# Optimization experiments

Measured on AMD Instinct MI355X. Metric: run time of the kernel, lower is better.

Reference implementation:

```python
import jax, jax.numpy as jnp
import numpy as np

INP = 64   # inplanes
PLN = 64   # planes
LOC = 64   # loc_planes
EPS = 1e-5


def _linear_init(key, fan_in, fan_out):
    # torch nn.Linear default: U(-1/sqrt(fan_in), 1/sqrt(fan_in)) for W and b
    kw, kb = jax.random.split(key)
    bound = 1.0 / np.sqrt(fan_in)
    W = jax.random.uniform(kw, (fan_in, fan_out), jnp.float32, -bound, bound)
    b = jax.random.uniform(kb, (fan_out,), jnp.float32, -bound, bound)
    return W, b


def setup_inputs() -> dict:
    key = jax.random.key(0)
    ks = jax.random.split(key, 8)
    B, N = 8, 4096
    img_fea = jax.random.normal(ks[0], (B, N, INP), jnp.float32)
    loc_fea = jax.random.normal(ks[1], (B, N, LOC), jnp.float32)
    W11, b11 = _linear_init(ks[2], INP + LOC, INP)
    W12, b12 = _linear_init(ks[3], INP, INP)
    W21, b21 = _linear_init(ks[4], INP + LOC, INP)
    W22, b22 = _linear_init(ks[5], INP, INP * PLN)
    W3, b3 = _linear_init(ks[6], PLN, PLN)
    ln_g = jnp.ones((PLN,), jnp.float32)
    ln_b = jnp.zeros((PLN,), jnp.float32)
    return {
        "img_fea": img_fea, "loc_fea": loc_fea,
        "W11": W11, "b11": b11, "W12": W12, "b12": b12,
        "W21": W21, "b21": b21, "W22": W22, "b22": b22,
        "ln_g": ln_g, "ln_b": ln_b, "W3": W3, "b3": b3,
    }


def reference(img_fea, loc_fea, W11, b11, W12, b12, W21, b21, W22, b22,
              ln_g, ln_b, W3, b3):
    B, N, C = img_fea.shape
    cat_fea = jnp.concatenate([img_fea, loc_fea], axis=2)  # [B,N,INP+LOC]
    # branch 1: per-token input vector
    w11 = jax.nn.relu(cat_fea @ W11 + b11)                 # [B,N,INP]
    w12 = w11 @ W12 + b12                                  # [B,N,INP]
    # branch 2: per-token weight matrix generation
    w21 = jax.nn.relu(cat_fea @ W21 + b21)                 # [B,N,INP]
    w22 = (w21 @ W22 + b22).reshape(B, N, INP, PLN)        # [B,N,INP,PLN]
    # batched tiny matvec: (1,INP) @ (INP,PLN) per token
    x = jnp.einsum('bni,bnio->bno', w12, w22)              # [B,N,PLN]
    # LayerNorm over last dim + ReLU
    mu = jnp.mean(x, axis=-1, keepdims=True)
    var = jnp.mean(jnp.square(x - mu), axis=-1, keepdims=True)
    x = (x - mu) * jax.lax.rsqrt(var + EPS) * ln_g + ln_b
    x = jax.nn.relu(x)
    # final linear (no activation)
    return x @ W3 + b3
```

## Files before the change

### kernel.cpp

```cpp
#include <hip/hip_runtime.h>
#include <cstdint>


typedef __bf16 bf16x8 __attribute__((ext_vector_type(8)));
typedef float  f32x4  __attribute__((ext_vector_type(4)));
typedef float  f32x8  __attribute__((ext_vector_type(8)));

#define MFMA16(A, B, C) __builtin_amdgcn_mfma_f32_16x16x32_bf16(A, B, C, 0, 0, 0)

#define OFF_BT22 0
#define OFF_W11  266240
#define OFF_W21  274432
#define OFF_W12  282624
#define OFF_W3   286720
#define WS_ELEMS 290816

__global__ __launch_bounds__(256) void prep_kernel(
    const float* __restrict__ W22, const float* __restrict__ b22,
    const float* __restrict__ W11, const float* __restrict__ W21,
    const float* __restrict__ W12, const float* __restrict__ W3,
    __bf16* __restrict__ ws)
{
    int gid = blockIdx.x * 256 + threadIdx.x;
    const float* src = nullptr; const float* srcb = nullptr;
    int base;
    if (gid < OFF_W11)      { base = OFF_BT22; src = W22; srcb = b22; }
    else if (gid < OFF_W12) { base = (gid < OFF_W21) ? OFF_W11 : OFF_W21;
                              src  = (gid < OFF_W21) ? W11 : W21; }
    else if (gid < OFF_W3)  { base = OFF_W12; src = W12; }
    else                    { base = OFF_W3;  src = W3;  }
    int d = gid - base;
    int kb = d >> 9, o = (d >> 3) & 63, kj = d & 7;
    int k = kb * 8 + kj;
    float v = (srcb && k >= 4096) ? srcb[(k - 4096) * 64 + o] : src[k * 64 + o];
    ws[gid] = (__bf16)v;
}

__global__ __launch_bounds__(256, 1) void main_kernel(
    const float* __restrict__ img, const float* __restrict__ loc,
    const float* __restrict__ b11, const float* __restrict__ b12,
    const float* __restrict__ b21, const float* __restrict__ ln_g,
    const float* __restrict__ ln_b, const float* __restrict__ b3,
    const __bf16* __restrict__ ws, float* __restrict__ out)
{
    __shared__ __align__(1024) char smem[90112];
    __bf16* catL = (__bf16*)smem;
    __bf16* w11L = (__bf16*)(smem + 34816);
    __bf16* w21L = (__bf16*)(smem + 53248);
    __bf16* w12L = (__bf16*)(smem + 71680);

    const int tid  = threadIdx.x;
    const int wv   = tid >> 6;
    const int lane = tid & 63;
    const int ln   = lane & 15;
    const int quad = lane >> 4;
    const int wt   = wv * 32;
    const long tb  = (long)blockIdx.x * 128;

    const __bf16* Bt22  = ws + OFF_BT22;
    const __bf16* W11bt = ws + OFF_W11;
    const __bf16* W21bt = ws + OFF_W21;
    const __bf16* W12bt = ws + OFF_W12;
    const __bf16* W3bt  = ws + OFF_W3;

    {
        const float* srcs[2] = {img, loc};
        #pragma unroll
        for (int s = 0; s < 2; ++s) {
            const float* src = srcs[s] + tb * 64;
            #pragma unroll
            for (int it = 0; it < 8; ++it) {
                int u = (it * 256 + tid) * 4;
                int t = u >> 6, c = u & 63;
                const float4 v = *(const float4*)(src + u);
                __bf16* p = catL + t * 136 + s * 64 + c;
                p[0] = (__bf16)v.x; p[1] = (__bf16)v.y;
                p[2] = (__bf16)v.z; p[3] = (__bf16)v.w;
            }
        }
    }
    __syncthreads();

    {
        f32x4 a11[2][4] = {}; f32x4 a21[2][4] = {};
        #pragma unroll
        for (int kb = 0; kb < 4; ++kb) {
            bf16x8 af[2];
            #pragma unroll
            for (int mf = 0; mf < 2; ++mf)
                af[mf] = *(const bf16x8*)(catL + (wt + mf*16 + ln)*136 + kb*32 + quad*8);
            #pragma unroll
            for (int nf = 0; nf < 4; ++nf) {
                int o = nf*16 + ln;
                bf16x8 bw1 = *(const bf16x8*)(W11bt + ((kb*4 + quad)*64 + o)*8);
                bf16x8 bw2 = *(const bf16x8*)(W21bt + ((kb*4 + quad)*64 + o)*8);
                #pragma unroll
                for (int mf = 0; mf < 2; ++mf) {
                    a11[mf][nf] = MFMA16(af[mf], bw1, a11[mf][nf]);
                    a21[mf][nf] = MFMA16(af[mf], bw2, a21[mf][nf]);
                }
            }
        }
        #pragma unroll
        for (int nf = 0; nf < 4; ++nf) {
            int o = nf*16 + ln;
            float c11 = b11[o], c21 = b21[o];
            #pragma unroll
            for (int mf = 0; mf < 2; ++mf)
                #pragma unroll
                for (int r = 0; r < 4; ++r) {
                    int t = wt + mf*16 + quad*4 + r;
                    float v1 = a11[mf][nf][r] + c11; v1 = v1 > 0.f ? v1 : 0.f;
                    float v2 = a21[mf][nf][r] + c21; v2 = v2 > 0.f ? v2 : 0.f;
                    w11L[t*72 + o] = (__bf16)v1;
                    w21L[t*72 + o] = (__bf16)v2;
                }
        }
    }
    __syncthreads();

    auto stage = [&](int c) {
        const int ng = (c == 32) ? 8 : 16;
        char* buf = smem + (c & 1) * 16384;
        for (int g = wv; g < ng; g += 4) {
            const __bf16* gsrc = Bt22 + ((long)(c*16 + g) * 512) + lane * 8;
            void* ldst = buf + g * 1024;
            __builtin_amdgcn_global_load_lds(
                (const __attribute__((address_space(1))) uint32_t*)gsrc,
                (__attribute__((address_space(3))) uint32_t*)ldst, 16, 0, 0);
        }
    };
    stage(0);

    {
        f32x4 a12c[2][4] = {};
        #pragma unroll
        for (int kb = 0; kb < 2; ++kb) {
            bf16x8 af[2];
            #pragma unroll
            for (int mf = 0; mf < 2; ++mf)
                af[mf] = *(const bf16x8*)(w11L + (wt + mf*16 + ln)*72 + kb*32 + quad*8);
            #pragma unroll
            for (int nf = 0; nf < 4; ++nf) {
                bf16x8 bw = *(const bf16x8*)(W12bt + ((kb*4 + quad)*64 + nf*16 + ln)*8);
                #pragma unroll
                for (int mf = 0; mf < 2; ++mf)
                    a12c[mf][nf] = MFMA16(af[mf], bw, a12c[mf][nf]);
            }
        }
        #pragma unroll
        for (int nf = 0; nf < 4; ++nf) {
            int o = nf*16 + ln;
            float c12 = b12[o];
            #pragma unroll
            for (int mf = 0; mf < 2; ++mf)
                #pragma unroll
                for (int r = 0; r < 4; ++r) {
                    int t = wt + mf*16 + quad*4 + r;
                    w12L[t*72 + o] = (__bf16)(a12c[mf][nf][r] + c12);
                }
        }
    }
    __syncthreads();

    bf16x8 a12[2][2]; f32x8 w12f[2][2];
    #pragma unroll
    for (int mf = 0; mf < 2; ++mf)
        #pragma unroll
        for (int sub = 0; sub < 2; ++sub) {
            a12[mf][sub]  = *(const bf16x8*)(w12L + (wt + mf*16 + ln)*72 + sub*32 + quad*8);
            w12f[mf][sub] = __builtin_convertvector(a12[mf][sub], f32x8);
        }

    f32x4 acc[2][4] = {};
    for (int c = 0; c <= 32; ++c) {
        if (c < 32) stage(c + 1);
        const __bf16* buf = (const __bf16*)(smem + (c & 1) * 16384);
        if (c < 32) {
            #pragma unroll
            for (int kbl = 0; kbl < 4; ++kbl) {
                int j = c*2 + (kbl >> 1), sub = kbl & 1;
                bf16x8 af[2];
                #pragma unroll
                for (int mf = 0; mf < 2; ++mf) {
                    float wj = (float)w21L[(wt + mf*16 + ln)*72 + j];
                    af[mf] = __builtin_convertvector(w12f[mf][sub] * wj, bf16x8);
                }
                #pragma unroll
                for (int nf = 0; nf < 4; ++nf) {
                    bf16x8 bfr = *(const bf16x8*)(buf + (kbl*4 + quad)*512 + (nf*16 + ln)*8);
                    #pragma unroll
                    for (int mf = 0; mf < 2; ++mf)
                        acc[mf][nf] = MFMA16(af[mf], bfr, acc[mf][nf]);
                }
            }
        } else {
            #pragma unroll
            for (int kbl = 0; kbl < 2; ++kbl)
                #pragma unroll
                for (int nf = 0; nf < 4; ++nf) {
                    bf16x8 bfr = *(const bf16x8*)(buf + (kbl*4 + quad)*512 + (nf*16 + ln)*8);
                    #pragma unroll
                    for (int mf = 0; mf < 2; ++mf)
                        acc[mf][nf] = MFMA16(a12[mf][kbl], bfr, acc[mf][nf]);
                }
        }
        __syncthreads();
    }

    float gv[4], bv[4], b3v[4];
    #pragma unroll
    for (int nf = 0; nf < 4; ++nf) {
        int o = nf*16 + ln;
        gv[nf] = ln_g[o]; bv[nf] = ln_b[o]; b3v[nf] = b3[o];
    }
    __bf16* xL = w11L;
    #pragma unroll
    for (int mf = 0; mf < 2; ++mf)
        #pragma unroll
        for (int r = 0; r < 4; ++r) {
            float s1 = 0.f, s2 = 0.f;
            #pragma unroll
            for (int nf = 0; nf < 4; ++nf) { float v = acc[mf][nf][r]; s1 += v; s2 += v*v; }
            #pragma unroll
            for (int d = 1; d < 16; d <<= 1) {
                s1 += __shfl_xor(s1, d, 64);
                s2 += __shfl_xor(s2, d, 64);
            }
            float mean = s1 * 0.015625f;
            float var  = s2 * 0.015625f - mean * mean;
            float inv  = rsqrtf(var + 1e-5f);
            int t = wt + mf*16 + quad*4 + r;
            #pragma unroll
            for (int nf = 0; nf < 4; ++nf) {
                float v = (acc[mf][nf][r] - mean) * inv * gv[nf] + bv[nf];
                v = v > 0.f ? v : 0.f;
                xL[t*72 + nf*16 + ln] = (__bf16)v;
            }
        }
    __syncthreads();

    f32x4 a3[2][4] = {};
    #pragma unroll
    for (int kb = 0; kb < 2; ++kb) {
        bf16x8 af[2];
        #pragma unroll
        for (int mf = 0; mf < 2; ++mf)
            af[mf] = *(const bf16x8*)(xL + (wt + mf*16 + ln)*72 + kb*32 + quad*8);
        #pragma unroll
        for (int nf = 0; nf < 4; ++nf) {
            bf16x8 bfr = *(const bf16x8*)(W3bt + ((kb*4 + quad)*64 + nf*16 + ln)*8);
            #pragma unroll
            for (int mf = 0; mf < 2; ++mf)
                a3[mf][nf] = MFMA16(af[mf], bfr, a3[mf][nf]);
        }
    }
    #pragma unroll
    for (int mf = 0; mf < 2; ++mf)
        #pragma unroll
        for (int nf = 0; nf < 4; ++nf)
            #pragma unroll
            for (int r = 0; r < 4; ++r) {
                long t = tb + wt + mf*16 + quad*4 + r;
                out[t*64 + nf*16 + ln] = a3[mf][nf][r] + b3v[nf];
            }
}

extern "C" void kernel_launch(void* const* d_in, const int* in_sizes, int n_in,
                              void* d_out, int out_size, void* d_ws, size_t ws_size,
                              hipStream_t stream)
{
    const float* img  = (const float*)d_in[0];
    const float* loc  = (const float*)d_in[1];
    const float* W11  = (const float*)d_in[2];
    const float* b11  = (const float*)d_in[3];
    const float* W12  = (const float*)d_in[4];
    const float* b12  = (const float*)d_in[5];
    const float* W21  = (const float*)d_in[6];
    const float* b21  = (const float*)d_in[7];
    const float* W22  = (const float*)d_in[8];
    const float* b22  = (const float*)d_in[9];
    const float* ln_g = (const float*)d_in[10];
    const float* ln_b = (const float*)d_in[11];
    const float* W3   = (const float*)d_in[12];
    const float* b3   = (const float*)d_in[13];
    __bf16* ws = (__bf16*)d_ws;
    float*  o  = (float*)d_out;

    prep_kernel<<<1136, 256, 0, stream>>>(W22, b22, W11, W21, W12, W3, ws);
    main_kernel<<<256, 256, 0, stream>>>(img, loc, b11, b12, b21, ln_g, ln_b, b3, ws, o);
}
```

Baseline: 134.9 us.

## Double W22 staging chunk size, tile prep transpose via LDS, vectorize stores

New measurement: 133.0 us. Within noise of the previous version (-1.3%).

```diff
diff --git a/kernel.cpp b/kernel.cpp
--- a/kernel.cpp
+++ b/kernel.cpp
@@ -2,6 +2,7 @@
 #include <cstdint>
 
 
+typedef __bf16 bf16x4 __attribute__((ext_vector_type(4)));
 typedef __bf16 bf16x8 __attribute__((ext_vector_type(8)));
 typedef float  f32x4  __attribute__((ext_vector_type(4)));
 typedef float  f32x8  __attribute__((ext_vector_type(8)));
@@ -13,7 +14,6 @@
 #define OFF_W21  274432
 #define OFF_W12  282624
 #define OFF_W3   286720
-#define WS_ELEMS 290816
 
 __global__ __launch_bounds__(256) void prep_kernel(
     const float* __restrict__ W22, const float* __restrict__ b22,
@@ -21,19 +21,33 @@
     const float* __restrict__ W12, const float* __restrict__ W3,
     __bf16* __restrict__ ws)
 {
-    int gid = blockIdx.x * 256 + threadIdx.x;
-    const float* src = nullptr; const float* srcb = nullptr;
-    int base;
-    if (gid < OFF_W11)      { base = OFF_BT22; src = W22; srcb = b22; }
-    else if (gid < OFF_W12) { base = (gid < OFF_W21) ? OFF_W11 : OFF_W21;
-                              src  = (gid < OFF_W21) ? W11 : W21; }
-    else if (gid < OFF_W3)  { base = OFF_W12; src = W12; }
-    else                    { base = OFF_W3;  src = W3;  }
-    int d = gid - base;
-    int kb = d >> 9, o = (d >> 3) & 63, kj = d & 7;
-    int k = kb * 8 + kj;
-    float v = (srcb && k >= 4096) ? srcb[(k - 4096) * 64 + o] : src[k * 64 + o];
-    ws[gid] = (__bf16)v;
+    __shared__ __bf16 T[64][72];
+    const int b = blockIdx.x, tid = threadIdx.x;
+    const float* src; __bf16* dst;
+    if (b < 64)       { src = W22 + b * 4096;        dst = ws + OFF_BT22 + b * 4096; }
+    else if (b == 64) { src = b22;                   dst = ws + OFF_BT22 + 64 * 4096; }
+    else if (b < 67)  { src = W11 + (b - 65) * 4096; dst = ws + OFF_W11 + (b - 65) * 4096; }
+    else if (b < 69)  { src = W21 + (b - 67) * 4096; dst = ws + OFF_W21 + (b - 67) * 4096; }
+    else if (b == 69) { src = W12;                   dst = ws + OFF_W12; }
+    else              { src = W3;                    dst = ws + OFF_W3; }
+    #pragma unroll
+    for (int it = 0; it < 4; ++it) {
+        int u = it * 1024 + tid * 4;
+        int r = u >> 6, c = u & 63;
+        const float4 v = *(const float4*)(src + u);
+        T[r][c] = (__bf16)v.x; T[r][c + 1] = (__bf16)v.y;
+        T[r][c + 2] = (__bf16)v.z; T[r][c + 3] = (__bf16)v.w;
+    }
+    __syncthreads();
+    #pragma unroll
+    for (int it = 0; it < 2; ++it) {
+        int item = it * 256 + tid;
+        int q = item >> 6, o = item & 63;
+        bf16x8 pk;
+        #pragma unroll
+        for (int kj = 0; kj < 8; ++kj) pk[kj] = T[q * 8 + kj][o];
+        *(bf16x8*)(dst + q * 512 + o * 8) = pk;
+    }
 }
 
 __global__ __launch_bounds__(256, 1) void main_kernel(
@@ -43,11 +57,11 @@
     const float* __restrict__ ln_b, const float* __restrict__ b3,
     const __bf16* __restrict__ ws, float* __restrict__ out)
 {
-    __shared__ __align__(1024) char smem[90112];
+    __shared__ __align__(1024) char smem[102400];
     __bf16* catL = (__bf16*)smem;
     __bf16* w11L = (__bf16*)(smem + 34816);
-    __bf16* w21L = (__bf16*)(smem + 53248);
-    __bf16* w12L = (__bf16*)(smem + 71680);
+    __bf16* w21L = (__bf16*)(smem + 65536);
+    __bf16* w12L = (__bf16*)(smem + 83968);
 
     const int tid  = threadIdx.x;
     const int wv   = tid >> 6;
@@ -73,9 +87,8 @@
                 int u = (it * 256 + tid) * 4;
                 int t = u >> 6, c = u & 63;
                 const float4 v = *(const float4*)(src + u);
-                __bf16* p = catL + t * 136 + s * 64 + c;
-                p[0] = (__bf16)v.x; p[1] = (__bf16)v.y;
-                p[2] = (__bf16)v.z; p[3] = (__bf16)v.w;
+                bf16x4 pk = {(__bf16)v.x, (__bf16)v.y, (__bf16)v.z, (__bf16)v.w};
+                *(bf16x4*)(catL + t * 136 + s * 64 + c) = pk;
             }
         }
     }
@@ -120,10 +133,10 @@
     __syncthreads();
 
     auto stage = [&](int c) {
-        const int ng = (c == 32) ? 8 : 16;
-        char* buf = smem + (c & 1) * 16384;
+        const int ng = (c == 16) ? 8 : 32;
+        char* buf = smem + (c & 1) * 32768;
         for (int g = wv; g < ng; g += 4) {
-            const __bf16* gsrc = Bt22 + ((long)(c*16 + g) * 512) + lane * 8;
+            const __bf16* gsrc = Bt22 + ((long)c * 16384 + g * 512) + lane * 8;
             void* ldst = buf + g * 1024;
             __builtin_amdgcn_global_load_lds(
                 (const __attribute__((address_space(1))) uint32_t*)gsrc,
@@ -173,22 +186,26 @@
         }
 
     f32x4 acc[2][4] = {};
-    for (int c = 0; c <= 32; ++c) {
-        if (c < 32) stage(c + 1);
-        const __bf16* buf = (const __bf16*)(smem + (c & 1) * 16384);
-        if (c < 32) {
-            #pragma unroll
-            for (int kbl = 0; kbl < 4; ++kbl) {
-                int j = c*2 + (kbl >> 1), sub = kbl & 1;
+    for (int c = 0; c <= 16; ++c) {
+        if (c < 16) stage(c + 1);
+        const __bf16* buf = (const __bf16*)(smem + (c & 1) * 32768);
+        if (c < 16) {
+            bf16x4 w21v[2];
+            #pragma unroll
+            for (int mf = 0; mf < 2; ++mf)
+                w21v[mf] = *(const bf16x4*)(w21L + (wt + mf*16 + ln)*72 + c*4);
+            #pragma unroll
+            for (int s = 0; s < 8; ++s) {
+                int sub = s & 1;
                 bf16x8 af[2];
                 #pragma unroll
                 for (int mf = 0; mf < 2; ++mf) {
-                    float wj = (float)w21L[(wt + mf*16 + ln)*72 + j];
+                    float wj = (float)w21v[mf][s >> 1];
                     af[mf] = __builtin_convertvector(w12f[mf][sub] * wj, bf16x8);
                 }
                 #pragma unroll
                 for (int nf = 0; nf < 4; ++nf) {
-                    bf16x8 bfr = *(const bf16x8*)(buf + (kbl*4 + quad)*512 + (nf*16 + ln)*8);
+                    bf16x8 bfr = *(const bf16x8*)(buf + (s*4 + quad)*512 + (nf*16 + ln)*8);
                     #pragma unroll
                     for (int mf = 0; mf < 2; ++mf)
                         acc[mf][nf] = MFMA16(af[mf], bfr, acc[mf][nf]);
@@ -196,13 +213,13 @@
             }
         } else {
             #pragma unroll
-            for (int kbl = 0; kbl < 2; ++kbl)
+            for (int s = 0; s < 2; ++s)
                 #pragma unroll
                 for (int nf = 0; nf < 4; ++nf) {
-                    bf16x8 bfr = *(const bf16x8*)(buf + (kbl*4 + quad)*512 + (nf*16 + ln)*8);
+                    bf16x8 bfr = *(const bf16x8*)(buf + (s*4 + quad)*512 + (nf*16 + ln)*8);
                     #pragma unroll
                     for (int mf = 0; mf < 2; ++mf)
-                        acc[mf][nf] = MFMA16(a12[mf][kbl], bfr, acc[mf][nf]);
+                        acc[mf][nf] = MFMA16(a12[mf][s], bfr, acc[mf][nf]);
                 }
         }
         __syncthreads();
@@ -214,7 +231,7 @@
         int o = nf*16 + ln;
         gv[nf] = ln_g[o]; bv[nf] = ln_b[o]; b3v[nf] = b3[o];
     }
-    __bf16* xL = w11L;
+    __bf16* xL = w12L;
     #pragma unroll
     for (int mf = 0; mf < 2; ++mf)
         #pragma unroll
@@ -287,6 +304,6 @@
     __bf16* ws = (__bf16*)d_ws;
     float*  o  = (float*)d_out;
 
-    prep_kernel<<<1136, 256, 0, stream>>>(W22, b22, W11, W21, W12, W3, ws);
+    prep_kernel<<<71, 256, 0, stream>>>(W22, b22, W11, W21, W12, W3, ws);
     main_kernel<<<256, 256, 0, stream>>>(img, loc, b11, b12, b21, ln_g, ln_b, b3, ws, o);
 }
```
